# Performance work log

Measured on AMD Instinct MI355X. Metric: run time of the kernel, lower is better.

## Reference

```python
import jax, jax.numpy as jnp
import numpy as np

B, L, D = 8, 2048, 512
H, P = 8, 4
C = D // H  # dim_per_head


def setup_inputs() -> dict:
    key = jax.random.key(0)
    ks = jax.random.split(key, 11)
    sc = lambda k, shape, s=0.02: jax.random.normal(k, shape, jnp.float32) * s
    return dict(
        query=jax.random.normal(ks[0], (B, L, D), jnp.float32),
        key_in=jax.random.normal(ks[1], (B, L, D), jnp.float32),
        value=jax.random.normal(ks[2], (B, L, D), jnp.float32),
        W_v=sc(ks[3], (D, D)), b_v=jnp.zeros((D,), jnp.float32),
        W_off=sc(ks[4], (D, H * P * 2), 0.01), b_off=sc(ks[5], (H * P * 2,), 0.2),
        W_aw=sc(ks[6], (D, H * P), 0.01), b_aw=jnp.zeros((H * P,), jnp.float32),
        W_out=sc(ks[7], (D, D)), b_out=jnp.zeros((D,), jnp.float32),
    )


def reference(query, key_in, value, W_v, b_v, W_off, b_off, W_aw, b_aw, W_out, b_out):
    # value projection
    v = value @ W_v + b_v                                        # (B,L,D)
    # sampling offsets and attention weights from the query
    off = (query @ W_off + b_off).reshape(B, L, H, P, 2)         # (B,L,H,P,2)
    aw = jax.nn.softmax((query @ W_aw + b_aw).reshape(B, L, H, P), axis=-1)
    # reference point for query i is (x=linspace[0]=0, y=linspace[i]) because
    # the torch code slices reference_points[:, :, :, :1, :]
    ref_y = jnp.linspace(0.0, 1.0, L, dtype=jnp.float32)
    loc_x = jnp.clip(off[..., 0], 0.0, 1.0)                      # ref_x = 0
    loc_y = jnp.clip(off[..., 1] + ref_y[None, :, None, None], 0.0, 1.0)
    # grid_sample, align_corners=False, input (BH, C, 1, L)
    ix = ((loc_x + 1.0) * L - 1.0) * 0.5                         # width coord in [ (L-1)/2, L-0.5 ]
    iy = loc_y * 0.5                                             # ((y+1)*1 - 1)/2
    ix0 = jnp.floor(ix)
    fx = ix - ix0
    iy0 = jnp.floor(iy)
    fy = iy - iy0
    # height dim has size 1: row iy0 valid iff ==0, row iy0+1 valid iff ==0 (zero padding)
    ywt = (1.0 - fy) * (iy0 == 0.0).astype(jnp.float32) + fy * ((iy0 + 1.0) == 0.0).astype(jnp.float32)
    i0 = ix0.astype(jnp.int32)
    i1 = i0 + 1

    perm = lambda a: a.transpose(0, 2, 1, 3)                     # (B,L,H,P) -> (B,H,L,P)
    i0p, i1p = perm(i0), perm(i1)
    vh = v.reshape(B, L, H, C).transpose(0, 2, 1, 3)             # (B,H,L,C)

    gather = jax.vmap(jax.vmap(lambda vm, ii: vm[ii]))           # (L,C),(L,P) -> (L,P,C)
    m0 = ((i0p >= 0) & (i0p < L)).astype(jnp.float32)[..., None]
    m1 = ((i1p >= 0) & (i1p < L)).astype(jnp.float32)[..., None]
    g0 = gather(vh, jnp.clip(i0p, 0, L - 1)) * m0                # (B,H,L,P,C)
    g1 = gather(vh, jnp.clip(i1p, 0, L - 1)) * m1

    fxp = perm(fx)[..., None]
    ywtp = perm(ywt)[..., None]
    samp = ywtp * ((1.0 - fxp) * g0 + fxp * g1)                  # (B,H,L,P,C)
    out = (samp * perm(aw)[..., None]).sum(axis=3)               # (B,H,L,C)
    out = out.transpose(0, 2, 1, 3).reshape(B, L, D)
    return out @ W_out + b_out
```

## Files before the change

### kernel.cpp

```cpp
#include <hip/hip_runtime.h>
#include <stdint.h>

#define PSZF (16384 * 96)

using short8  = __attribute__((ext_vector_type(8))) short;
using floatx4 = __attribute__((ext_vector_type(4))) float;

__device__ __forceinline__ unsigned short f2bf(float f) {
  union { float f; unsigned u; } v; v.f = f;
  unsigned r = v.u + 0x7fffu + ((v.u >> 16) & 1u);
  return (unsigned short)(r >> 16);
}
__device__ __forceinline__ float bf2f(unsigned short u) {
  union { unsigned u; float f; } v; v.u = ((unsigned)u) << 16; return v.f;
}

__device__ __forceinline__ void load_lds16(const void* g, void* l) {
  __builtin_amdgcn_global_load_lds(
      (const __attribute__((address_space(1))) unsigned int*)g,
      (__attribute__((address_space(3))) unsigned int*)l, 16, 0, 0);
}

__device__ __forceinline__ void store_val(float* p, float v) { *p = v; }
__device__ __forceinline__ void store_val(unsigned short* p, float v) { *p = f2bf(v); }

__global__ __launch_bounds__(256) void prep_all(const float* __restrict__ value,
                                                const float* __restrict__ W_v,
                                                const float* __restrict__ W_out,
                                                const float* __restrict__ Woff,
                                                const float* __restrict__ Waw,
                                                const float* __restrict__ boff,
                                                const float* __restrict__ baw,
                                                unsigned short* __restrict__ val_bf,
                                                unsigned short* __restrict__ Wv_t,
                                                unsigned short* __restrict__ Wo_t,
                                                unsigned short* __restrict__ Bhi,
                                                unsigned short* __restrict__ Blo,
                                                float* __restrict__ bcat) {
  int idx = blockIdx.x * 256 + threadIdx.x;
  if (idx < 2097152) {
    float4 v = ((const float4*)value)[idx];
    ushort4 o;
    o.x = f2bf(v.x); o.y = f2bf(v.y); o.z = f2bf(v.z); o.w = f2bf(v.w);
    ((ushort4*)val_bf)[idx] = o;
    return;
  }
  int t = idx - 2097152;
  if (t < 262144) {
    int n = t >> 9, k = t & 511;
    Wv_t[t] = f2bf(W_v[(k << 9) + n]);
    return;
  }
  t -= 262144;
  if (t < 262144) {
    int n = t >> 9, k = t & 511;
    Wo_t[t] = f2bf(W_out[(k << 9) + n]);
    return;
  }
  t -= 262144;
  if (t < 49152) {
    int n = t >> 9, k = t & 511;
    float w = (n < 64) ? Woff[(k << 6) + n] : Waw[(k << 5) + (n - 64)];
    unsigned short hi = f2bf(w);
    Bhi[t] = hi;
    Blo[t] = f2bf(w - bf2f(hi));
    return;
  }
  t -= 49152;
  if (t < 96) bcat[t] = (t < 64) ? boff[t] : baw[t - 64];
}

template <typename OutT>
__device__ __forceinline__ void gemm_body(unsigned char* smem,
                                          const unsigned short* __restrict__ A,
                                          const unsigned short* __restrict__ Bt,
                                          const float* __restrict__ bias,
                                          OutT* __restrict__ C, int N, int K,
                                          int bx, int by) {
  unsigned short* lA = (unsigned short*)smem;
  unsigned short* lB = (unsigned short*)(smem + 8192);
  int tid  = threadIdx.x;
  int lane = tid & 63, wv = tid >> 6;
  int wm = wv & 1, wn = wv >> 1;
  int lrow = lane & 15, quad = lane >> 4;
  int rowBlk = by * 128, colBlk = bx * 128;

  const unsigned short* Ab = A + (size_t)rowBlk * K;
  const unsigned short* Bb = Bt + (size_t)colBlk * K;
  int r0 = tid >> 2;
  int c0 = (tid & 3) << 3;

  floatx4 acc[4][4];
#pragma unroll
  for (int i = 0; i < 4; i++)
#pragma unroll
    for (int j = 0; j < 4; j++) acc[i][j] = (floatx4){0.f, 0.f, 0.f, 0.f};

  for (int k0 = 0; k0 < K; k0 += 32) {
    load_lds16(Ab + (size_t)r0 * K + k0 + c0,        lA + tid * 8);
    load_lds16(Ab + (size_t)(r0 + 64) * K + k0 + c0, lA + 2048 + tid * 8);
    load_lds16(Bb + (size_t)r0 * K + k0 + c0,        lB + tid * 8);
    load_lds16(Bb + (size_t)(r0 + 64) * K + k0 + c0, lB + 2048 + tid * 8);
    __syncthreads();

    short8 a[4], b[4];
#pragma unroll
    for (int mi = 0; mi < 4; mi++)
      a[mi] = *(const short8*)&lA[(wm * 64 + mi * 16 + lrow) * 32 + quad * 8];
#pragma unroll
    for (int ni = 0; ni < 4; ni++)
      b[ni] = *(const short8*)&lB[(wn * 64 + ni * 16 + lrow) * 32 + quad * 8];
#pragma unroll
    for (int mi = 0; mi < 4; mi++)
#pragma unroll
      for (int ni = 0; ni < 4; ni++)
        acc[mi][ni] = __builtin_amdgcn_mfma_f32_16x16x32_bf16(a[mi], b[ni], acc[mi][ni], 0, 0, 0);
    __syncthreads();
  }

#pragma unroll
  for (int ni = 0; ni < 4; ni++) {
    int col = colBlk + wn * 64 + ni * 16 + lrow;
    float bv = bias[col];
#pragma unroll
    for (int mi = 0; mi < 4; mi++) {
      int row = rowBlk + wm * 64 + mi * 16 + quad * 4;
#pragma unroll
      for (int r = 0; r < 4; r++)
        store_val(&C[(size_t)(row + r) * N + col], acc[mi][ni][r] + bv);
    }
  }
}

__device__ __forceinline__ void offaw_body(unsigned char* smem,
                                           const float* __restrict__ Q,
                                           const unsigned short* __restrict__ Bhi,
                                           const unsigned short* __restrict__ Blo,
                                           const float* __restrict__ bcat,
                                           float* __restrict__ P, int bid) {
  unsigned short* lAhi = (unsigned short*)smem;
  unsigned short* lAlo = (unsigned short*)(smem + 4096);
  unsigned short* lBhi = (unsigned short*)(smem + 8192);
  unsigned short* lBlo = (unsigned short*)(smem + 14336);
  int khalf = bid >> 8, row0 = (bid & 255) * 64, kbase = khalf << 8;
  int tid = threadIdx.x, lane = tid & 63, wv = tid >> 6;
  int wm = wv & 1, wn = wv >> 1, lrow = lane & 15, quad = lane >> 4;

  int ar = tid >> 2, ac = (tid & 3) << 3;
  const float* qp = Q + (size_t)(row0 + ar) * 512 + kbase + ac;

  floatx4 acc[2][3];
#pragma unroll
  for (int i = 0; i < 2; i++)
#pragma unroll
    for (int j = 0; j < 3; j++) acc[i][j] = (floatx4){0.f, 0.f, 0.f, 0.f};

  for (int k0 = 0; k0 < 256; k0 += 32) {
    float4 v0 = *(const float4*)(qp + k0);
    float4 v1 = *(const float4*)(qp + k0 + 4);
    float vv[8] = {v0.x, v0.y, v0.z, v0.w, v1.x, v1.y, v1.z, v1.w};
    short8 h8, l8;
#pragma unroll
    for (int e = 0; e < 8; e++) {
      union { float f; unsigned u; } t; t.f = vv[e];
      unsigned r = t.u + 0x7fffu + ((t.u >> 16) & 1u);
      h8[e] = (short)(r >> 16);
      union { unsigned u; float f; } hf; hf.u = r & 0xffff0000u;
      union { float f; unsigned u; } rb; rb.f = vv[e] - hf.f;
      l8[e] = (short)(rb.u >> 16);
    }
    *(short8*)&lAhi[tid * 8] = h8;
    *(short8*)&lAlo[tid * 8] = l8;
#pragma unroll
    for (int j = 0; j < 3; j++) {
      int widx = wv + (j << 2);
      const unsigned short* src = (widx < 6) ? Bhi : Blo;
      unsigned short* dst = (widx < 6) ? lBhi : lBlo;
      int c = (((widx < 6) ? widx : widx - 6) << 6) + lane;
      int n = c >> 2, cc = (c & 3) << 3;
      load_lds16(src + (size_t)n * 512 + kbase + k0 + cc, dst + c * 8);
    }
    __syncthreads();

    short8 ah[2], al[2], bh[3], bl[3];
#pragma unroll
    for (int mi = 0; mi < 2; mi++) {
      int r = (wm * 32 + mi * 16 + lrow) * 32 + quad * 8;
      ah[mi] = *(const short8*)&lAhi[r];
      al[mi] = *(const short8*)&lAlo[r];
    }
#pragma unroll
    for (int ni = 0; ni < 3; ni++) {
      int r = (wn * 48 + ni * 16 + lrow) * 32 + quad * 8;
      bh[ni] = *(const short8*)&lBhi[r];
      bl[ni] = *(const short8*)&lBlo[r];
    }
#pragma unroll
    for (int mi = 0; mi < 2; mi++)
#pragma unroll
      for (int ni = 0; ni < 3; ni++) {
        acc[mi][ni] = __builtin_amdgcn_mfma_f32_16x16x32_bf16(ah[mi], bh[ni], acc[mi][ni], 0, 0, 0);
        acc[mi][ni] = __builtin_amdgcn_mfma_f32_16x16x32_bf16(ah[mi], bl[ni], acc[mi][ni], 0, 0, 0);
        acc[mi][ni] = __builtin_amdgcn_mfma_f32_16x16x32_bf16(al[mi], bh[ni], acc[mi][ni], 0, 0, 0);
      }
    __syncthreads();
  }

  float* out = P + (size_t)khalf * PSZF;
#pragma unroll
  for (int ni = 0; ni < 3; ni++) {
    int col = wn * 48 + ni * 16 + lrow;
    float bv = (khalf == 0) ? bcat[col] : 0.0f;
#pragma unroll
    for (int mi = 0; mi < 2; mi++) {
      int row = row0 + wm * 32 + mi * 16 + quad * 4;
#pragma unroll
      for (int r = 0; r < 4; r++)
        out[(size_t)(row + r) * 96 + col] = acc[mi][ni][r] + bv;
    }
  }
}

__global__ __launch_bounds__(256) void mega_k2(const unsigned short* __restrict__ val_bf,
                                               const unsigned short* __restrict__ Wv_t,
                                               const float* __restrict__ b_v,
                                               unsigned short* __restrict__ v_bf,
                                               const float* __restrict__ query,
                                               const unsigned short* __restrict__ Bhi,
                                               const unsigned short* __restrict__ Blo,
                                               const float* __restrict__ bcat,
                                               float* __restrict__ offP) {
  __shared__ __align__(16) unsigned char smem[20480];
  int bx = blockIdx.x;
  if (bx < 512)
    gemm_body<unsigned short>(smem, val_bf, Wv_t, b_v, v_bf, 512, 512, bx & 3, bx >> 2);
  else
    offaw_body(smem, query, Bhi, Blo, bcat, offP, bx - 512);
}

__global__ __launch_bounds__(256) void gemm2_k(const unsigned short* __restrict__ A,
                                               const unsigned short* __restrict__ Bt,
                                               const float* __restrict__ bias,
                                               float* __restrict__ C) {
  __shared__ __align__(16) unsigned char smem[16384];
  gemm_body<float>(smem, A, Bt, bias, C, 512, 512, blockIdx.x & 3, blockIdx.x >> 2);
}

__global__ __launch_bounds__(256) void sample_kernel(const float* __restrict__ P,
                                                     const unsigned short* __restrict__ v,
                                                     unsigned short* __restrict__ attn) {
  int row = blockIdx.x;
  int b = row >> 11, l = row & 2047;
  __shared__ float s_w0[32], s_w1[32];
  __shared__ int s_i0[32], s_i1[32];
  int tid = threadIdx.x;

  if (tid < 32) {
    int base = row * 96;
    float lg = P[base + 64 + tid] + P[PSZF + base + 64 + tid];
    float mx = fmaxf(lg, __shfl_xor(lg, 1));
    mx = fmaxf(mx, __shfl_xor(mx, 2));
    float e = __expf(lg - mx);
    float s = e + __shfl_xor(e, 1);
    s = s + __shfl_xor(s, 2);
    float aw = e / s;

    float ox = P[base + 2 * tid] + P[PSZF + base + 2 * tid];
    float oy = P[base + 2 * tid + 1] + P[PSZF + base + 2 * tid + 1];
    float refy = (float)l * (1.0f / 2047.0f);
    float lx = fminf(fmaxf(ox, 0.0f), 1.0f);
    float ly = fminf(fmaxf(oy + refy, 0.0f), 1.0f);
    float ix = ((lx + 1.0f) * 2048.0f - 1.0f) * 0.5f;
    float ywt = 1.0f - ly * 0.5f;
    float ix0 = floorf(ix);
    float fx = ix - ix0;
    int i0 = (int)ix0;
    int i1 = i0 + 1;
    s_w0[tid] = aw * ywt * (1.0f - fx);
    s_w1[tid] = (i1 < 2048) ? (aw * ywt * fx) : 0.0f;
    s_i0[tid] = i0;
    s_i1[tid] = (i1 < 2048) ? i1 : 2047;
  }
  __syncthreads();

  const unsigned short* vb = v + ((size_t)(b << 11)) * 512;
  int h = tid >> 5, c = (tid & 31) << 1;
  const unsigned short* vhc = vb + h * 64 + c;
  float ax = 0.0f, ay = 0.0f;
#pragma unroll
  for (int p = 0; p < 4; p++) {
    int t = (h << 2) + p;
    unsigned g0 = *(const unsigned*)(vhc + ((size_t)s_i0[t] << 9));
    unsigned g1 = *(const unsigned*)(vhc + ((size_t)s_i1[t] << 9));
    float w0 = s_w0[t], w1 = s_w1[t];
    ax += w0 * bf2f((unsigned short)g0) + w1 * bf2f((unsigned short)g1);
    ay += w0 * bf2f((unsigned short)(g0 >> 16)) + w1 * bf2f((unsigned short)(g1 >> 16));
  }
  unsigned packed = (unsigned)f2bf(ax) | ((unsigned)f2bf(ay) << 16);
  *(unsigned*)(attn + (size_t)row * 512 + h * 64 + c) = packed;
}

extern "C" void kernel_launch(void* const* d_in, const int* in_sizes, int n_in,
                              void* d_out, int out_size, void* d_ws, size_t ws_size,
                              hipStream_t stream) {
  (void)in_sizes; (void)n_in; (void)out_size; (void)ws_size;
  const float* query = (const float*)d_in[0];
  const float* value = (const float*)d_in[2];
  const float* W_v   = (const float*)d_in[3];
  const float* b_v   = (const float*)d_in[4];
  const float* W_off = (const float*)d_in[5];
  const float* b_off = (const float*)d_in[6];
  const float* W_aw  = (const float*)d_in[7];
  const float* b_aw  = (const float*)d_in[8];
  const float* W_out = (const float*)d_in[9];
  const float* b_out = (const float*)d_in[10];
  float* out = (float*)d_out;

  char* ws = (char*)d_ws;
  const size_t MB = 1ull << 20;
  unsigned short* val_bf = (unsigned short*)(ws);
  unsigned short* attn   = val_bf;
  unsigned short* v_bf   = (unsigned short*)(ws + 16 * MB);
  float* offP            = (float*)(ws + 32 * MB);
  unsigned short* Wv_t   = (unsigned short*)(ws + 48 * MB);
  unsigned short* Wo_t   = (unsigned short*)(ws + 48 * MB + 524288);
  unsigned short* Bhi    = (unsigned short*)(ws + 49 * MB);
  unsigned short* Blo    = (unsigned short*)(ws + 49 * MB + 98304);
  float* bcat            = (float*)(ws + 49 * MB + 196608);

  prep_all<<<10433, 256, 0, stream>>>(value, W_v, W_out, W_off, W_aw, b_off, b_aw,
                                      val_bf, Wv_t, Wo_t, Bhi, Blo, bcat);
  mega_k2<<<1024, 256, 0, stream>>>(val_bf, Wv_t, b_v, v_bf, query, Bhi, Blo, bcat, offP);
  sample_kernel<<<16384, 256, 0, stream>>>(offP, v_bf, attn);
  gemm2_k<<<512, 256, 0, stream>>>(attn, Wo_t, b_out, out);
}
```

Baseline: 206.8 us.

## Fuse value bf16 conversion into V-projection GEMM and retile GEMMs and sampling

```diff
diff --git a/kernel.cpp b/kernel.cpp
--- a/kernel.cpp
+++ b/kernel.cpp
@@ -24,34 +24,24 @@
 __device__ __forceinline__ void store_val(float* p, float v) { *p = v; }
 __device__ __forceinline__ void store_val(unsigned short* p, float v) { *p = f2bf(v); }
 
-__global__ __launch_bounds__(256) void prep_all(const float* __restrict__ value,
-                                                const float* __restrict__ W_v,
-                                                const float* __restrict__ W_out,
-                                                const float* __restrict__ Woff,
-                                                const float* __restrict__ Waw,
-                                                const float* __restrict__ boff,
-                                                const float* __restrict__ baw,
-                                                unsigned short* __restrict__ val_bf,
-                                                unsigned short* __restrict__ Wv_t,
-                                                unsigned short* __restrict__ Wo_t,
-                                                unsigned short* __restrict__ Bhi,
-                                                unsigned short* __restrict__ Blo,
-                                                float* __restrict__ bcat) {
+__global__ __launch_bounds__(256) void prep_w(const float* __restrict__ W_v,
+                                              const float* __restrict__ W_out,
+                                              const float* __restrict__ Woff,
+                                              const float* __restrict__ Waw,
+                                              const float* __restrict__ boff,
+                                              const float* __restrict__ baw,
+                                              unsigned short* __restrict__ Wv_t,
+                                              unsigned short* __restrict__ Wo_t,
+                                              unsigned short* __restrict__ Bhi,
+                                              unsigned short* __restrict__ Blo,
+                                              float* __restrict__ bcat) {
   int idx = blockIdx.x * 256 + threadIdx.x;
-  if (idx < 2097152) {
-    float4 v = ((const float4*)value)[idx];
-    ushort4 o;
-    o.x = f2bf(v.x); o.y = f2bf(v.y); o.z = f2bf(v.z); o.w = f2bf(v.w);
-    ((ushort4*)val_bf)[idx] = o;
+  if (idx < 262144) {
+    int n = idx >> 9, k = idx & 511;
+    Wv_t[idx] = f2bf(W_v[(k << 9) + n]);
     return;
   }
-  int t = idx - 2097152;
-  if (t < 262144) {
-    int n = t >> 9, k = t & 511;
-    Wv_t[t] = f2bf(W_v[(k << 9) + n]);
-    return;
-  }
-  t -= 262144;
+  int t = idx - 262144;
   if (t < 262144) {
     int n = t >> 9, k = t & 511;
     Wo_t[t] = f2bf(W_out[(k << 9) + n]);
@@ -71,63 +61,115 @@
 }
 
 template <typename OutT>
-__device__ __forceinline__ void gemm_body(unsigned char* smem,
-                                          const unsigned short* __restrict__ A,
-                                          const unsigned short* __restrict__ Bt,
-                                          const float* __restrict__ bias,
-                                          OutT* __restrict__ C, int N, int K,
-                                          int bx, int by) {
-  unsigned short* lA = (unsigned short*)smem;
-  unsigned short* lB = (unsigned short*)(smem + 8192);
+__device__ __forceinline__ void gemm64_body(unsigned short* lA, unsigned short* lB,
+                                            const unsigned short* __restrict__ A,
+                                            const unsigned short* __restrict__ Bt,
+                                            const float* __restrict__ bias,
+                                            OutT* __restrict__ C, int bx, int by) {
   int tid  = threadIdx.x;
   int lane = tid & 63, wv = tid >> 6;
   int wm = wv & 1, wn = wv >> 1;
   int lrow = lane & 15, quad = lane >> 4;
-  int rowBlk = by * 128, colBlk = bx * 128;
-
-  const unsigned short* Ab = A + (size_t)rowBlk * K;
-  const unsigned short* Bb = Bt + (size_t)colBlk * K;
-  int r0 = tid >> 2;
-  int c0 = (tid & 3) << 3;
-
-  floatx4 acc[4][4];
-#pragma unroll
-  for (int i = 0; i < 4; i++)
-#pragma unroll
-    for (int j = 0; j < 4; j++) acc[i][j] = (floatx4){0.f, 0.f, 0.f, 0.f};
-
-  for (int k0 = 0; k0 < K; k0 += 32) {
-    load_lds16(Ab + (size_t)r0 * K + k0 + c0,        lA + tid * 8);
-    load_lds16(Ab + (size_t)(r0 + 64) * K + k0 + c0, lA + 2048 + tid * 8);
-    load_lds16(Bb + (size_t)r0 * K + k0 + c0,        lB + tid * 8);
-    load_lds16(Bb + (size_t)(r0 + 64) * K + k0 + c0, lB + 2048 + tid * 8);
-    __syncthreads();
-
-    short8 a[4], b[4];
-#pragma unroll
-    for (int mi = 0; mi < 4; mi++)
-      a[mi] = *(const short8*)&lA[(wm * 64 + mi * 16 + lrow) * 32 + quad * 8];
-#pragma unroll
-    for (int ni = 0; ni < 4; ni++)
-      b[ni] = *(const short8*)&lB[(wn * 64 + ni * 16 + lrow) * 32 + quad * 8];
-#pragma unroll
-    for (int mi = 0; mi < 4; mi++)
-#pragma unroll
-      for (int ni = 0; ni < 4; ni++)
+  int rowBlk = by * 64, colBlk = bx * 64;
+  const unsigned short* Ab = A + (size_t)rowBlk * 512;
+  const unsigned short* Bb = Bt + (size_t)colBlk * 512;
+  int r0 = tid >> 2, c0 = (tid & 3) << 3;
+
+  floatx4 acc[2][2];
+#pragma unroll
+  for (int i = 0; i < 2; i++)
+#pragma unroll
+    for (int j = 0; j < 2; j++) acc[i][j] = (floatx4){0.f, 0.f, 0.f, 0.f};
+
+  for (int k0 = 0; k0 < 512; k0 += 32) {
+    load_lds16(Ab + (size_t)r0 * 512 + k0 + c0, lA + tid * 8);
+    load_lds16(Bb + (size_t)r0 * 512 + k0 + c0, lB + tid * 8);
+    __syncthreads();
+    short8 a[2], b[2];
+#pragma unroll
+    for (int mi = 0; mi < 2; mi++)
+      a[mi] = *(const short8*)&lA[(wm * 32 + mi * 16 + lrow) * 32 + quad * 8];
+#pragma unroll
+    for (int ni = 0; ni < 2; ni++)
+      b[ni] = *(const short8*)&lB[(wn * 32 + ni * 16 + lrow) * 32 + quad * 8];
+#pragma unroll
+    for (int mi = 0; mi < 2; mi++)
+#pragma unroll
+      for (int ni = 0; ni < 2; ni++)
         acc[mi][ni] = __builtin_amdgcn_mfma_f32_16x16x32_bf16(a[mi], b[ni], acc[mi][ni], 0, 0, 0);
     __syncthreads();
   }
 
 #pragma unroll
-  for (int ni = 0; ni < 4; ni++) {
-    int col = colBlk + wn * 64 + ni * 16 + lrow;
+  for (int ni = 0; ni < 2; ni++) {
+    int col = colBlk + wn * 32 + ni * 16 + lrow;
     float bv = bias[col];
 #pragma unroll
-    for (int mi = 0; mi < 4; mi++) {
-      int row = rowBlk + wm * 64 + mi * 16 + quad * 4;
+    for (int mi = 0; mi < 2; mi++) {
+      int row = rowBlk + wm * 32 + mi * 16 + quad * 4;
 #pragma unroll
       for (int r = 0; r < 4; r++)
-        store_val(&C[(size_t)(row + r) * N + col], acc[mi][ni][r] + bv);
+        store_val(&C[(size_t)(row + r) * 512 + col], acc[mi][ni][r] + bv);
+    }
+  }
+}
+
+__device__ __forceinline__ void gemm1_body(unsigned short* lA, unsigned short* lB,
+                                           const float* __restrict__ A,
+                                           const unsigned short* __restrict__ Bt,
+                                           const float* __restrict__ bias,
+                                           unsigned short* __restrict__ C,
+                                           int bx, int by) {
+  int tid  = threadIdx.x;
+  int lane = tid & 63, wv = tid >> 6;
+  int wm = wv & 1, wn = wv >> 1;
+  int lrow = lane & 15, quad = lane >> 4;
+  int rowBlk = by * 64, colBlk = bx * 64;
+  const unsigned short* Bb = Bt + (size_t)colBlk * 512;
+  int r0 = tid >> 2, c0 = (tid & 3) << 3;
+  const float* ap = A + (size_t)(rowBlk + r0) * 512 + c0;
+
+  floatx4 acc[2][2];
+#pragma unroll
+  for (int i = 0; i < 2; i++)
+#pragma unroll
+    for (int j = 0; j < 2; j++) acc[i][j] = (floatx4){0.f, 0.f, 0.f, 0.f};
+
+  for (int k0 = 0; k0 < 512; k0 += 32) {
+    float4 v0 = *(const float4*)(ap + k0);
+    float4 v1 = *(const float4*)(ap + k0 + 4);
+    float vv[8] = {v0.x, v0.y, v0.z, v0.w, v1.x, v1.y, v1.z, v1.w};
+    short8 h8;
+#pragma unroll
+    for (int e = 0; e < 8; e++) h8[e] = (short)f2bf(vv[e]);
+    *(short8*)&lA[tid * 8] = h8;
+    load_lds16(Bb + (size_t)r0 * 512 + k0 + c0, lB + tid * 8);
+    __syncthreads();
+    short8 a[2], b[2];
+#pragma unroll
+    for (int mi = 0; mi < 2; mi++)
+      a[mi] = *(const short8*)&lA[(wm * 32 + mi * 16 + lrow) * 32 + quad * 8];
+#pragma unroll
+    for (int ni = 0; ni < 2; ni++)
+      b[ni] = *(const short8*)&lB[(wn * 32 + ni * 16 + lrow) * 32 + quad * 8];
+#pragma unroll
+    for (int mi = 0; mi < 2; mi++)
+#pragma unroll
+      for (int ni = 0; ni < 2; ni++)
+        acc[mi][ni] = __builtin_amdgcn_mfma_f32_16x16x32_bf16(a[mi], b[ni], acc[mi][ni], 0, 0, 0);
+    __syncthreads();
+  }
+
+#pragma unroll
+  for (int ni = 0; ni < 2; ni++) {
+    int col = colBlk + wn * 32 + ni * 16 + lrow;
+    float bv = bias[col];
+#pragma unroll
+    for (int mi = 0; mi < 2; mi++) {
+      int row = rowBlk + wm * 32 + mi * 16 + quad * 4;
+#pragma unroll
+      for (int r = 0; r < 4; r++)
+        C[(size_t)(row + r) * 512 + col] = f2bf(acc[mi][ni][r] + bv);
     }
   }
 }
@@ -221,7 +263,7 @@
   }
 }
 
-__global__ __launch_bounds__(256) void mega_k2(const unsigned short* __restrict__ val_bf,
+__global__ __launch_bounds__(256) void mega_k1(const float* __restrict__ value,
                                                const unsigned short* __restrict__ Wv_t,
                                                const float* __restrict__ b_v,
                                                unsigned short* __restrict__ v_bf,
@@ -232,32 +274,34 @@
                                                float* __restrict__ offP) {
   __shared__ __align__(16) unsigned char smem[20480];
   int bx = blockIdx.x;
-  if (bx < 512)
-    gemm_body<unsigned short>(smem, val_bf, Wv_t, b_v, v_bf, 512, 512, bx & 3, bx >> 2);
+  if (bx < 2048)
+    gemm1_body((unsigned short*)smem, (unsigned short*)(smem + 4096),
+               value, Wv_t, b_v, v_bf, bx & 7, bx >> 3);
   else
-    offaw_body(smem, query, Bhi, Blo, bcat, offP, bx - 512);
+    offaw_body(smem, query, Bhi, Blo, bcat, offP, bx - 2048);
 }
 
 __global__ __launch_bounds__(256) void gemm2_k(const unsigned short* __restrict__ A,
                                                const unsigned short* __restrict__ Bt,
                                                const float* __restrict__ bias,
                                                float* __restrict__ C) {
-  __shared__ __align__(16) unsigned char smem[16384];
-  gemm_body<float>(smem, A, Bt, bias, C, 512, 512, blockIdx.x & 3, blockIdx.x >> 2);
+  __shared__ __align__(16) unsigned short lA[2048];
+  __shared__ __align__(16) unsigned short lB[2048];
+  gemm64_body<float>(lA, lB, A, Bt, bias, C, blockIdx.x & 7, blockIdx.x >> 3);
 }
 
 __global__ __launch_bounds__(256) void sample_kernel(const float* __restrict__ P,
                                                      const unsigned short* __restrict__ v,
                                                      unsigned short* __restrict__ attn) {
-  int row = blockIdx.x;
-  int b = row >> 11, l = row & 2047;
-  __shared__ float s_w0[32], s_w1[32];
-  __shared__ int s_i0[32], s_i1[32];
   int tid = threadIdx.x;
-
-  if (tid < 32) {
+  int rr = tid >> 5, hp = tid & 31;
+  int row = blockIdx.x * 8 + rr;
+  int l = row & 2047;
+  __shared__ float s_w0[8][32], s_w1[8][32];
+  __shared__ int s_i0[8][32], s_i1[8][32];
+  {
     int base = row * 96;
-    float lg = P[base + 64 + tid] + P[PSZF + base + 64 + tid];
+    float lg = P[base + 64 + hp] + P[PSZF + base + 64 + hp];
     float mx = fmaxf(lg, __shfl_xor(lg, 1));
     mx = fmaxf(mx, __shfl_xor(mx, 2));
     float e = __expf(lg - mx);
@@ -265,8 +309,8 @@
     s = s + __shfl_xor(s, 2);
     float aw = e / s;
 
-    float ox = P[base + 2 * tid] + P[PSZF + base + 2 * tid];
-    float oy = P[base + 2 * tid + 1] + P[PSZF + base + 2 * tid + 1];
+    float ox = P[base + 2 * hp] + P[PSZF + base + 2 * hp];
+    float oy = P[base + 2 * hp + 1] + P[PSZF + base + 2 * hp + 1];
     float refy = (float)l * (1.0f / 2047.0f);
     float lx = fminf(fmaxf(ox, 0.0f), 1.0f);
     float ly = fminf(fmaxf(oy + refy, 0.0f), 1.0f);
@@ -276,28 +320,32 @@
     float fx = ix - ix0;
     int i0 = (int)ix0;
     int i1 = i0 + 1;
-    s_w0[tid] = aw * ywt * (1.0f - fx);
-    s_w1[tid] = (i1 < 2048) ? (aw * ywt * fx) : 0.0f;
-    s_i0[tid] = i0;
-    s_i1[tid] = (i1 < 2048) ? i1 : 2047;
+    s_w0[rr][hp] = aw * ywt * (1.0f - fx);
+    s_w1[rr][hp] = (i1 < 2048) ? (aw * ywt * fx) : 0.0f;
+    s_i0[rr][hp] = i0;
+    s_i1[rr][hp] = (i1 < 2048) ? i1 : 2047;
   }
   __syncthreads();
 
-  const unsigned short* vb = v + ((size_t)(b << 11)) * 512;
+  int b = (blockIdx.x * 8) >> 11;
   int h = tid >> 5, c = (tid & 31) << 1;
-  const unsigned short* vhc = vb + h * 64 + c;
-  float ax = 0.0f, ay = 0.0f;
-#pragma unroll
-  for (int p = 0; p < 4; p++) {
-    int t = (h << 2) + p;
-    unsigned g0 = *(const unsigned*)(vhc + ((size_t)s_i0[t] << 9));
-    unsigned g1 = *(const unsigned*)(vhc + ((size_t)s_i1[t] << 9));
-    float w0 = s_w0[t], w1 = s_w1[t];
-    ax += w0 * bf2f((unsigned short)g0) + w1 * bf2f((unsigned short)g1);
-    ay += w0 * bf2f((unsigned short)(g0 >> 16)) + w1 * bf2f((unsigned short)(g1 >> 16));
-  }
-  unsigned packed = (unsigned)f2bf(ax) | ((unsigned)f2bf(ay) << 16);
-  *(unsigned*)(attn + (size_t)row * 512 + h * 64 + c) = packed;
+  const unsigned short* vhc = v + ((size_t)(b << 11)) * 512 + h * 64 + c;
+#pragma unroll
+  for (int r8 = 0; r8 < 8; r8++) {
+    int row2 = blockIdx.x * 8 + r8;
+    float ax = 0.0f, ay = 0.0f;
+#pragma unroll
+    for (int p = 0; p < 4; p++) {
+      int t = (h << 2) + p;
+      unsigned g0 = *(const unsigned*)(vhc + ((size_t)s_i0[r8][t] << 9));
+      unsigned g1 = *(const unsigned*)(vhc + ((size_t)s_i1[r8][t] << 9));
+      float w0 = s_w0[r8][t], w1 = s_w1[r8][t];
+      ax += w0 * bf2f((unsigned short)g0) + w1 * bf2f((unsigned short)g1);
+      ay += w0 * bf2f((unsigned short)(g0 >> 16)) + w1 * bf2f((unsigned short)(g1 >> 16));
+    }
+    unsigned packed = (unsigned)f2bf(ax) | ((unsigned)f2bf(ay) << 16);
+    *(unsigned*)(attn + (size_t)row2 * 512 + h * 64 + c) = packed;
+  }
 }
 
 extern "C" void kernel_launch(void* const* d_in, const int* in_sizes, int n_in,
@@ -318,19 +366,18 @@
 
   char* ws = (char*)d_ws;
   const size_t MB = 1ull << 20;
-  unsigned short* val_bf = (unsigned short*)(ws);
-  unsigned short* attn   = val_bf;
-  unsigned short* v_bf   = (unsigned short*)(ws + 16 * MB);
-  float* offP            = (float*)(ws + 32 * MB);
-  unsigned short* Wv_t   = (unsigned short*)(ws + 48 * MB);
-  unsigned short* Wo_t   = (unsigned short*)(ws + 48 * MB + 524288);
-  unsigned short* Bhi    = (unsigned short*)(ws + 49 * MB);
-  unsigned short* Blo    = (unsigned short*)(ws + 49 * MB + 98304);
-  float* bcat            = (float*)(ws + 49 * MB + 196608);
-
-  prep_all<<<10433, 256, 0, stream>>>(value, W_v, W_out, W_off, W_aw, b_off, b_aw,
-                                      val_bf, Wv_t, Wo_t, Bhi, Blo, bcat);
-  mega_k2<<<1024, 256, 0, stream>>>(val_bf, Wv_t, b_v, v_bf, query, Bhi, Blo, bcat, offP);
-  sample_kernel<<<16384, 256, 0, stream>>>(offP, v_bf, attn);
-  gemm2_k<<<512, 256, 0, stream>>>(attn, Wo_t, b_out, out);
-}
+  unsigned short* v_bf = (unsigned short*)(ws);
+  unsigned short* attn = (unsigned short*)(ws + 16 * MB);
+  float* offP          = (float*)(ws + 32 * MB);
+  unsigned short* Wv_t = (unsigned short*)(ws + 48 * MB);
+  unsigned short* Wo_t = (unsigned short*)(ws + 48 * MB + 524288);
+  unsigned short* Bhi  = (unsigned short*)(ws + 49 * MB);
+  unsigned short* Blo  = (unsigned short*)(ws + 49 * MB + 98304);
+  float* bcat          = (float*)(ws + 49 * MB + 196608);
+
+  prep_w<<<2241, 256, 0, stream>>>(W_v, W_out, W_off, W_aw, b_off, b_aw,
+                                   Wv_t, Wo_t, Bhi, Blo, bcat);
+  mega_k1<<<2560, 256, 0, stream>>>(value, Wv_t, b_v, v_bf, query, Bhi, Blo, bcat, offP);
+  sample_kernel<<<2048, 256, 0, stream>>>(offP, v_bf, attn);
+  gemm2_k<<<2048, 256, 0, stream>>>(attn, Wo_t, b_out, out);
+}
```

After: 221.0 us. 1.07x slower.

## Deepen GEMM K-step, swizzle block order, batch 8 rows per sample block

Applied to the files above, without the earlier changes.

```diff
diff --git a/kernel.cpp b/kernel.cpp
--- a/kernel.cpp
+++ b/kernel.cpp
@@ -71,22 +71,21 @@
 }
 
 template <typename OutT>
-__device__ __forceinline__ void gemm_body(unsigned char* smem,
-                                          const unsigned short* __restrict__ A,
-                                          const unsigned short* __restrict__ Bt,
-                                          const float* __restrict__ bias,
-                                          OutT* __restrict__ C, int N, int K,
-                                          int bx, int by) {
+__device__ __forceinline__ void gemm_body64(unsigned char* smem,
+                                            const unsigned short* __restrict__ A,
+                                            const unsigned short* __restrict__ Bt,
+                                            const float* __restrict__ bias,
+                                            OutT* __restrict__ C, int bx, int by) {
   unsigned short* lA = (unsigned short*)smem;
-  unsigned short* lB = (unsigned short*)(smem + 8192);
+  unsigned short* lB = (unsigned short*)(smem + 16384);
   int tid  = threadIdx.x;
   int lane = tid & 63, wv = tid >> 6;
   int wm = wv & 1, wn = wv >> 1;
   int lrow = lane & 15, quad = lane >> 4;
   int rowBlk = by * 128, colBlk = bx * 128;
 
-  const unsigned short* Ab = A + (size_t)rowBlk * K;
-  const unsigned short* Bb = Bt + (size_t)colBlk * K;
+  const unsigned short* Ab = A + (size_t)rowBlk * 512;
+  const unsigned short* Bb = Bt + (size_t)colBlk * 512;
   int r0 = tid >> 2;
   int c0 = (tid & 3) << 3;
 
@@ -96,25 +95,32 @@
 #pragma unroll
     for (int j = 0; j < 4; j++) acc[i][j] = (floatx4){0.f, 0.f, 0.f, 0.f};
 
-  for (int k0 = 0; k0 < K; k0 += 32) {
-    load_lds16(Ab + (size_t)r0 * K + k0 + c0,        lA + tid * 8);
-    load_lds16(Ab + (size_t)(r0 + 64) * K + k0 + c0, lA + 2048 + tid * 8);
-    load_lds16(Bb + (size_t)r0 * K + k0 + c0,        lB + tid * 8);
-    load_lds16(Bb + (size_t)(r0 + 64) * K + k0 + c0, lB + 2048 + tid * 8);
+  for (int k0 = 0; k0 < 512; k0 += 64) {
+    load_lds16(Ab + (size_t)r0 * 512 + k0 + c0,             lA + tid * 8);
+    load_lds16(Ab + (size_t)(r0 + 64) * 512 + k0 + c0,      lA + 2048 + tid * 8);
+    load_lds16(Bb + (size_t)r0 * 512 + k0 + c0,             lB + tid * 8);
+    load_lds16(Bb + (size_t)(r0 + 64) * 512 + k0 + c0,      lB + 2048 + tid * 8);
+    load_lds16(Ab + (size_t)r0 * 512 + k0 + 32 + c0,        lA + 4096 + tid * 8);
+    load_lds16(Ab + (size_t)(r0 + 64) * 512 + k0 + 32 + c0, lA + 6144 + tid * 8);
+    load_lds16(Bb + (size_t)r0 * 512 + k0 + 32 + c0,        lB + 4096 + tid * 8);
+    load_lds16(Bb + (size_t)(r0 + 64) * 512 + k0 + 32 + c0, lB + 6144 + tid * 8);
     __syncthreads();
 
-    short8 a[4], b[4];
-#pragma unroll
-    for (int mi = 0; mi < 4; mi++)
-      a[mi] = *(const short8*)&lA[(wm * 64 + mi * 16 + lrow) * 32 + quad * 8];
-#pragma unroll
-    for (int ni = 0; ni < 4; ni++)
-      b[ni] = *(const short8*)&lB[(wn * 64 + ni * 16 + lrow) * 32 + quad * 8];
-#pragma unroll
-    for (int mi = 0; mi < 4; mi++)
+#pragma unroll
+    for (int kc = 0; kc < 2; kc++) {
+      short8 a[4], b[4];
+#pragma unroll
+      for (int mi = 0; mi < 4; mi++)
+        a[mi] = *(const short8*)&lA[kc * 4096 + (wm * 64 + mi * 16 + lrow) * 32 + quad * 8];
 #pragma unroll
       for (int ni = 0; ni < 4; ni++)
-        acc[mi][ni] = __builtin_amdgcn_mfma_f32_16x16x32_bf16(a[mi], b[ni], acc[mi][ni], 0, 0, 0);
+        b[ni] = *(const short8*)&lB[kc * 4096 + (wn * 64 + ni * 16 + lrow) * 32 + quad * 8];
+#pragma unroll
+      for (int mi = 0; mi < 4; mi++)
+#pragma unroll
+        for (int ni = 0; ni < 4; ni++)
+          acc[mi][ni] = __builtin_amdgcn_mfma_f32_16x16x32_bf16(a[mi], b[ni], acc[mi][ni], 0, 0, 0);
+    }
     __syncthreads();
   }
 
@@ -127,9 +133,15 @@
       int row = rowBlk + wm * 64 + mi * 16 + quad * 4;
 #pragma unroll
       for (int r = 0; r < 4; r++)
-        store_val(&C[(size_t)(row + r) * N + col], acc[mi][ni][r] + bv);
-    }
-  }
+        store_val(&C[(size_t)(row + r) * 512 + col], acc[mi][ni][r] + bv);
+    }
+  }
+}
+
+__device__ __forceinline__ void swz512(int bid, int& bx, int& by) {
+  int x = bid & 7, s = bid >> 3;
+  by = (x << 4) | (s >> 2);
+  bx = s & 3;
 }
 
 __device__ __forceinline__ void offaw_body(unsigned char* smem,
@@ -221,7 +233,7 @@
   }
 }
 
-__global__ __launch_bounds__(256) void mega_k2(const unsigned short* __restrict__ val_bf,
+__global__ __launch_bounds__(256) void mega_k1(const unsigned short* __restrict__ val_bf,
                                                const unsigned short* __restrict__ Wv_t,
                                                const float* __restrict__ b_v,
                                                unsigned short* __restrict__ v_bf,
@@ -230,34 +242,37 @@
                                                const unsigned short* __restrict__ Blo,
                                                const float* __restrict__ bcat,
                                                float* __restrict__ offP) {
-  __shared__ __align__(16) unsigned char smem[20480];
-  int bx = blockIdx.x;
-  if (bx < 512)
-    gemm_body<unsigned short>(smem, val_bf, Wv_t, b_v, v_bf, 512, 512, bx & 3, bx >> 2);
-  else
-    offaw_body(smem, query, Bhi, Blo, bcat, offP, bx - 512);
+  __shared__ __align__(16) unsigned char smem[32768];
+  int bid = blockIdx.x;
+  if (bid < 512) {
+    int bx, by; swz512(bid, bx, by);
+    gemm_body64<unsigned short>(smem, val_bf, Wv_t, b_v, v_bf, bx, by);
+  } else {
+    offaw_body(smem, query, Bhi, Blo, bcat, offP, bid - 512);
+  }
 }
 
 __global__ __launch_bounds__(256) void gemm2_k(const unsigned short* __restrict__ A,
                                                const unsigned short* __restrict__ Bt,
                                                const float* __restrict__ bias,
                                                float* __restrict__ C) {
-  __shared__ __align__(16) unsigned char smem[16384];
-  gemm_body<float>(smem, A, Bt, bias, C, 512, 512, blockIdx.x & 3, blockIdx.x >> 2);
+  __shared__ __align__(16) unsigned char smem[32768];
+  int bx, by; swz512(blockIdx.x, bx, by);
+  gemm_body64<float>(smem, A, Bt, bias, C, bx, by);
 }
 
 __global__ __launch_bounds__(256) void sample_kernel(const float* __restrict__ P,
                                                      const unsigned short* __restrict__ v,
                                                      unsigned short* __restrict__ attn) {
-  int row = blockIdx.x;
-  int b = row >> 11, l = row & 2047;
-  __shared__ float s_w0[32], s_w1[32];
-  __shared__ int s_i0[32], s_i1[32];
   int tid = threadIdx.x;
-
-  if (tid < 32) {
+  int rr = tid >> 5, hp = tid & 31;
+  int row = blockIdx.x * 8 + rr;
+  int l = row & 2047;
+  __shared__ float s_w0[8][32], s_w1[8][32];
+  __shared__ int s_i0[8][32], s_i1[8][32];
+  {
     int base = row * 96;
-    float lg = P[base + 64 + tid] + P[PSZF + base + 64 + tid];
+    float lg = P[base + 64 + hp] + P[PSZF + base + 64 + hp];
     float mx = fmaxf(lg, __shfl_xor(lg, 1));
     mx = fmaxf(mx, __shfl_xor(mx, 2));
     float e = __expf(lg - mx);
@@ -265,8 +280,8 @@
     s = s + __shfl_xor(s, 2);
     float aw = e / s;
 
-    float ox = P[base + 2 * tid] + P[PSZF + base + 2 * tid];
-    float oy = P[base + 2 * tid + 1] + P[PSZF + base + 2 * tid + 1];
+    float ox = P[base + 2 * hp] + P[PSZF + base + 2 * hp];
+    float oy = P[base + 2 * hp + 1] + P[PSZF + base + 2 * hp + 1];
     float refy = (float)l * (1.0f / 2047.0f);
     float lx = fminf(fmaxf(ox, 0.0f), 1.0f);
     float ly = fminf(fmaxf(oy + refy, 0.0f), 1.0f);
@@ -276,28 +291,32 @@
     float fx = ix - ix0;
     int i0 = (int)ix0;
     int i1 = i0 + 1;
-    s_w0[tid] = aw * ywt * (1.0f - fx);
-    s_w1[tid] = (i1 < 2048) ? (aw * ywt * fx) : 0.0f;
-    s_i0[tid] = i0;
-    s_i1[tid] = (i1 < 2048) ? i1 : 2047;
+    s_w0[rr][hp] = aw * ywt * (1.0f - fx);
+    s_w1[rr][hp] = (i1 < 2048) ? (aw * ywt * fx) : 0.0f;
+    s_i0[rr][hp] = i0;
+    s_i1[rr][hp] = (i1 < 2048) ? i1 : 2047;
   }
   __syncthreads();
 
-  const unsigned short* vb = v + ((size_t)(b << 11)) * 512;
+  int b = (blockIdx.x * 8) >> 11;
   int h = tid >> 5, c = (tid & 31) << 1;
-  const unsigned short* vhc = vb + h * 64 + c;
-  float ax = 0.0f, ay = 0.0f;
-#pragma unroll
-  for (int p = 0; p < 4; p++) {
-    int t = (h << 2) + p;
-    unsigned g0 = *(const unsigned*)(vhc + ((size_t)s_i0[t] << 9));
-    unsigned g1 = *(const unsigned*)(vhc + ((size_t)s_i1[t] << 9));
-    float w0 = s_w0[t], w1 = s_w1[t];
-    ax += w0 * bf2f((unsigned short)g0) + w1 * bf2f((unsigned short)g1);
-    ay += w0 * bf2f((unsigned short)(g0 >> 16)) + w1 * bf2f((unsigned short)(g1 >> 16));
-  }
-  unsigned packed = (unsigned)f2bf(ax) | ((unsigned)f2bf(ay) << 16);
-  *(unsigned*)(attn + (size_t)row * 512 + h * 64 + c) = packed;
+  const unsigned short* vhc = v + ((size_t)(b << 11)) * 512 + h * 64 + c;
+#pragma unroll
+  for (int r8 = 0; r8 < 8; r8++) {
+    int row2 = blockIdx.x * 8 + r8;
+    float ax = 0.0f, ay = 0.0f;
+#pragma unroll
+    for (int p = 0; p < 4; p++) {
+      int t = (h << 2) + p;
+      unsigned g0 = *(const unsigned*)(vhc + ((size_t)s_i0[r8][t] << 9));
+      unsigned g1 = *(const unsigned*)(vhc + ((size_t)s_i1[r8][t] << 9));
+      float w0 = s_w0[r8][t], w1 = s_w1[r8][t];
+      ax += w0 * bf2f((unsigned short)g0) + w1 * bf2f((unsigned short)g1);
+      ay += w0 * bf2f((unsigned short)(g0 >> 16)) + w1 * bf2f((unsigned short)(g1 >> 16));
+    }
+    unsigned packed = (unsigned)f2bf(ax) | ((unsigned)f2bf(ay) << 16);
+    *(unsigned*)(attn + (size_t)row2 * 512 + h * 64 + c) = packed;
+  }
 }
 
 extern "C" void kernel_launch(void* const* d_in, const int* in_sizes, int n_in,
@@ -330,7 +349,7 @@
 
   prep_all<<<10433, 256, 0, stream>>>(value, W_v, W_out, W_off, W_aw, b_off, b_aw,
                                       val_bf, Wv_t, Wo_t, Bhi, Blo, bcat);
-  mega_k2<<<1024, 256, 0, stream>>>(val_bf, Wv_t, b_v, v_bf, query, Bhi, Blo, bcat, offP);
-  sample_kernel<<<16384, 256, 0, stream>>>(offP, v_bf, attn);
+  mega_k1<<<1024, 256, 0, stream>>>(val_bf, Wv_t, b_v, v_bf, query, Bhi, Blo, bcat, offP);
+  sample_kernel<<<2048, 256, 0, stream>>>(offP, v_bf, attn);
   gemm2_k<<<512, 256, 0, stream>>>(attn, Wo_t, b_out, out);
 }
```

Measured after the change: 192.3 us. 1.08x faster.
